# Optimization experiments

Measured on AMD Instinct MI355X. Metric: run time of the kernel, lower is better.

Reference implementation:

```python
import jax, jax.numpy as jnp
import numpy as np

B, S, DIM = 2, 2048, 2048
N_HEADS, N_KV_HEADS = 16, 4
HEAD_DIM = DIM // N_HEADS  # 128
N_REP = N_HEADS // N_KV_HEADS
ROPE_THETA = 10000.0


def _rope_cos_sin(bsz, seqlen, head_dim, theta):
    # precompute_freqs_cis (unscaled): angles[t, i] = t * theta^{-2i/d}
    inv_freq = 1.0 / (theta ** (np.arange(0, head_dim, 2)[: head_dim // 2].astype(np.float32) / head_dim))
    t = np.arange(seqlen, dtype=np.float32)
    ang = np.outer(t, inv_freq)  # [S, hd/2]
    cos = np.broadcast_to(np.cos(ang), (bsz, seqlen, head_dim // 2))
    sin = np.broadcast_to(np.sin(ang), (bsz, seqlen, head_dim // 2))
    return jnp.asarray(cos), jnp.asarray(sin)


def setup_inputs() -> dict:
    key = jax.random.key(0)
    ks = jax.random.split(key, 5)
    scale = 1.0 / np.sqrt(DIM)
    x = jax.random.normal(ks[0], (B, S, DIM), dtype=jnp.float32)
    wq = jax.random.normal(ks[1], (DIM, N_HEADS * HEAD_DIM), dtype=jnp.float32) * scale
    wk = jax.random.normal(ks[2], (DIM, N_KV_HEADS * HEAD_DIM), dtype=jnp.float32) * scale
    wv = jax.random.normal(ks[3], (DIM, N_KV_HEADS * HEAD_DIM), dtype=jnp.float32) * scale
    wo = jax.random.normal(ks[4], (N_HEADS * HEAD_DIM, DIM), dtype=jnp.float32) * scale
    freqs_cos, freqs_sin = _rope_cos_sin(B, S, HEAD_DIM, ROPE_THETA)
    return {"x": x, "wq": wq, "wk": wk, "wv": wv, "wo": wo,
            "freqs_cos": freqs_cos, "freqs_sin": freqs_sin}


def _apply_rope(t, cos, sin):
    # t: [B, S, H, hd]; cos/sin: [B, S, hd/2] -> complex mult on (even, odd) pairs
    tr = t.reshape(*t.shape[:-1], -1, 2)  # [B,S,H,hd/2,2]
    xr, xi = tr[..., 0], tr[..., 1]
    c = cos[:, :, None, :]
    s = sin[:, :, None, :]
    out_r = xr * c - xi * s
    out_i = xr * s + xi * c
    return jnp.stack([out_r, out_i], axis=-1).reshape(t.shape)


def reference(x, wq, wk, wv, wo, freqs_cos, freqs_sin):
    bsz, seqlen, _ = x.shape
    xq = (x @ wq).reshape(bsz, seqlen, N_HEADS, HEAD_DIM)
    xk = (x @ wk).reshape(bsz, seqlen, N_KV_HEADS, HEAD_DIM)
    xv = (x @ wv).reshape(bsz, seqlen, N_KV_HEADS, HEAD_DIM)

    xq = _apply_rope(xq, freqs_cos, freqs_sin)
    xk = _apply_rope(xk, freqs_cos, freqs_sin)

    # repeat_kv (GQA): [B,S,KV,hd] -> [B,S,H,hd]
    xk = jnp.repeat(xk, N_REP, axis=2)
    xv = jnp.repeat(xv, N_REP, axis=2)

    # [B,H,Sq,Sk]
    scores = jnp.einsum('bqhd,bkhd->bhqk', xq, xk) / np.sqrt(HEAD_DIM).astype(np.float32)
    # additive causal mask (triu of -inf, diagonal=1)
    causal = jnp.triu(jnp.full((seqlen, seqlen), -jnp.inf, dtype=scores.dtype), k=1)
    scores = scores + causal
    probs = jax.nn.softmax(scores.astype(jnp.float32), axis=-1).astype(xq.dtype)
    out = jnp.einsum('bhqk,bkhd->bqhd', probs, xv).reshape(bsz, seqlen, -1)
    return out @ wo
```

## Files before the change

kernel.cpp:

```cpp
#include <hip/hip_runtime.h>
#include <stdint.h>

#define SEQ   2048
#define NB    2
#define LDQKV 3072
#define HD    128
#define QSCALE2 (0.08838834764831845f * 1.44269504088896340f)

typedef __attribute__((ext_vector_type(8))) short short8;
typedef __attribute__((ext_vector_type(4))) short short4v;
typedef __attribute__((ext_vector_type(4))) float f32x4;
typedef __attribute__((ext_vector_type(16))) float f32x16;
typedef __attribute__((ext_vector_type(4))) unsigned int u32x4;
typedef __attribute__((ext_vector_type(2))) unsigned int u32x2;
typedef __attribute__((ext_vector_type(8))) __bf16 bf16x8;

__device__ __forceinline__ float bs2f(short s) {
  unsigned int u = ((unsigned int)(unsigned short)s) << 16;
  return __builtin_bit_cast(float, u);
}
__device__ __forceinline__ short f2bs(float f) {
  unsigned int u = __builtin_bit_cast(unsigned int, f);
  u += 0x7fffu + ((u >> 16) & 1u);
  return (short)(u >> 16);
}
__device__ __forceinline__ unsigned int cvt_pk(float lo, float hi) {
  unsigned int r;
  asm("v_cvt_pk_bf16_f32 %0, %1, %2" : "=v"(r) : "v"(lo), "v"(hi));
  return r;
}
__device__ __forceinline__ f32x4 mfma16(short8 a, short8 b, f32x4 c) {
  return __builtin_amdgcn_mfma_f32_16x16x32_bf16(
      __builtin_bit_cast(bf16x8, a), __builtin_bit_cast(bf16x8, b), c, 0, 0, 0);
}
__device__ __forceinline__ f32x16 mfma32(short8 a, short8 b, f32x16 c) {
  return __builtin_amdgcn_mfma_f32_32x32x16_bf16(
      __builtin_bit_cast(bf16x8, a), __builtin_bit_cast(bf16x8, b), c, 0, 0, 0);
}
__device__ __forceinline__ void gload_lds16(const void* g, void* l) {
  __builtin_amdgcn_global_load_lds(
      (__attribute__((address_space(1))) const void*)(uintptr_t)g,
      (__attribute__((address_space(3))) void*)(unsigned int)(uintptr_t)l,
      16, 0, 0);
}

#define SBAR() asm volatile("s_barrier" ::: "memory")
#define VMC4() asm volatile("s_waitcnt vmcnt(4)" ::: "memory")
#define VMC0() asm volatile("s_waitcnt vmcnt(0)" ::: "memory")

__global__ __launch_bounds__(256) void k_prep(const float* __restrict__ x,
                                              const float* __restrict__ wq,
                                              const float* __restrict__ wk,
                                              const float* __restrict__ wv,
                                              const float* __restrict__ wo,
                                              short* __restrict__ xb,
                                              short* __restrict__ wT,
                                              short* __restrict__ woT) {
  __shared__ __align__(16) float tile[64][68];
  const int bid = blockIdx.x, t = threadIdx.x;
  if (bid < 4096) {
    int i = bid * 256 + t;
    f32x4 a = *(const f32x4*)(x + (size_t)i * 8);
    f32x4 b = *(const f32x4*)(x + (size_t)i * 8 + 4);
    short8 o;
#pragma unroll
    for (int j = 0; j < 4; ++j) { o[j] = f2bs(a[j]); o[4 + j] = f2bs(b[j]); }
    *(short8*)(xb + (size_t)i * 8) = o;
    return;
  }
  const float* src;
  short* dst;
  int N, id;
  if (bid < 5120)      { id = bid - 4096; src = wq; dst = wT;                        N = 2048; }
  else if (bid < 5376) { id = bid - 5120; src = wk; dst = wT + (size_t)2048 * 2048;  N = 512;  }
  else if (bid < 5632) { id = bid - 5376; src = wv; dst = wT + (size_t)2560 * 2048;  N = 512;  }
  else                 { id = bid - 5632; src = wo; dst = woT;                       N = 2048; }
  const int K = 2048;
  int k0 = (id & 31) * 64, n0 = (id >> 5) * 64;
#pragma unroll
  for (int rep = 0; rep < 4; ++rep) {
    int lin = rep * 1024 + t * 4;
    int kk = lin >> 6, nn = lin & 63;
    f32x4 v = *(const f32x4*)(src + (size_t)(k0 + kk) * N + n0 + nn);
    *(f32x4*)(&tile[kk][nn]) = v;
  }
  __syncthreads();
#pragma unroll
  for (int rep = 0; rep < 4; ++rep) {
    int lin = rep * 1024 + t * 4;
    int nn = lin >> 6, kk = lin & 63;
    short4v o;
#pragma unroll
    for (int j = 0; j < 4; ++j) o[j] = f2bs(tile[kk + j][nn]);
    *(short4v*)(dst + (size_t)(n0 + nn) * K + k0 + kk) = o;
  }
}

template <int FP32OUT>
__global__ __launch_bounds__(512, 2) void k_gemm256(const short* __restrict__ A,
                                                    const short* __restrict__ Bt,
                                                    void* __restrict__ Cp,
                                                    int M, int N, int K) {
  __shared__ short Al[2][2][128 * 64];
  __shared__ short Bl[2][2][128 * 64];
  const int t = threadIdx.x, l = t & 63, w = t >> 6;
  const int pm = w >> 2, pn = w & 3;
  const int lrow = l & 15, lg = l >> 4;
  const int NT = K >> 6;

  const int nbm = M >> 8;
  const int per = gridDim.x >> 3;
  const int id2 = (blockIdx.x & 7) * per + (blockIdx.x >> 3);
  const int m0 = (id2 % nbm) * 256, n0 = (id2 / nbm) * 256;

  const int srow = w * 8 + (l >> 3);
  const int sgx = ((l & 7) ^ (srow & 7)) * 8;
  const short* Abase = A + (size_t)(m0 + srow) * K + sgx;
  const short* Bbase = Bt + (size_t)(n0 + srow) * K + sgx;

  f32x4 acc[8][4] = {};
  short8 aFr[4][2], bFr[2][2];

  auto stgA = [&](int d, int h, int tv) {
    const short* g = Abase + (size_t)(h * 128) * K + (size_t)tv * 64;
    gload_lds16(g, &Al[d][h][w * 512]);
    gload_lds16(g + (size_t)64 * K, &Al[d][h][w * 512 + 4096]);
  };
  auto stgB = [&](int d, int h, int tv) {
    const short* g = Bbase + (size_t)(h * 128) * K + (size_t)tv * 64;
    gload_lds16(g, &Bl[d][h][w * 512]);
    gload_lds16(g + (size_t)64 * K, &Bl[d][h][w * 512 + 4096]);
  };
  auto rdA = [&](int d, int Mh) {
#pragma unroll
    for (int mi = 0; mi < 4; ++mi) {
      int rl = pm * 64 + mi * 16 + lrow;
#pragma unroll
      for (int kk = 0; kk < 2; ++kk)
        aFr[mi][kk] = *(const short8*)&Al[d][Mh][rl * 64 +
                                                 (((kk * 4 + lg) ^ (rl & 7)) * 8)];
    }
  };
  auto rdB = [&](int d, int Nh) {
#pragma unroll
    for (int ni = 0; ni < 2; ++ni) {
      int rl = pn * 32 + ni * 16 + lrow;
#pragma unroll
      for (int kk = 0; kk < 2; ++kk)
        bFr[ni][kk] = *(const short8*)&Bl[d][Nh][rl * 64 +
                                                 (((kk * 4 + lg) ^ (rl & 7)) * 8)];
    }
  };

#define MMQ(Mh, Nh)                                                          \
  do {                                                                       \
    __builtin_amdgcn_s_setprio(1);                                           \
    _Pragma("unroll") for (int mi = 0; mi < 4; ++mi)                         \
        _Pragma("unroll") for (int ni = 0; ni < 2; ++ni)                     \
            _Pragma("unroll") for (int kk = 0; kk < 2; ++kk)                 \
                acc[(Mh)*4 + mi][(Nh)*2 + ni] =                              \
                    mfma16(aFr[mi][kk], bFr[ni][kk],                         \
                           acc[(Mh)*4 + mi][(Nh)*2 + ni]);                   \
    __builtin_amdgcn_s_setprio(0);                                           \
  } while (0)

  stgA(0, 0, 0); stgB(0, 0, 0); stgB(0, 1, 0); stgA(0, 1, 0);
  stgA(1, 0, 1); stgB(1, 1, 1);
  VMC4();
  SBAR();

  for (int v = 0; v < NT; ++v) {
    const int d = v & 1, d1 = d ^ 1;
    rdA(d, 0); rdB(d, 0);
    if (v + 1 < NT) stgB(d1, 0, v + 1);
    SBAR();
    MMQ(0, 0);
    rdB(d, 1);
    if (v + 1 < NT) stgA(d1, 1, v + 1);
    SBAR();
    MMQ(0, 1);
    rdA(d, 1);
    if (v + 2 < NT) stgA(d, 0, v + 2);
    SBAR();
    MMQ(1, 1);
    rdB(d, 0);
    if (v + 2 < NT) stgB(d, 1, v + 2);
    SBAR();
    MMQ(1, 0);
    if (v + 2 < NT) { VMC4(); } else { VMC0(); }
    SBAR();
  }
#undef MMQ

#pragma unroll
  for (int Mh = 0; Mh < 2; ++Mh)
#pragma unroll
    for (int mi = 0; mi < 4; ++mi)
#pragma unroll
      for (int Nh = 0; Nh < 2; ++Nh)
#pragma unroll
        for (int ni = 0; ni < 2; ++ni) {
          int row = m0 + Mh * 128 + pm * 64 + mi * 16 + lg * 4;
          int col = n0 + Nh * 128 + pn * 32 + ni * 16 + lrow;
          f32x4 vv = acc[Mh * 4 + mi][Nh * 2 + ni];
#pragma unroll
          for (int v2 = 0; v2 < 4; ++v2) {
            if constexpr (FP32OUT)
              ((float*)Cp)[(size_t)(row + v2) * N + col] = vv[v2];
            else
              ((short*)Cp)[(size_t)(row + v2) * N + col] = f2bs(vv[v2]);
          }
        }
}

__global__ __launch_bounds__(256) void k_rv(short* __restrict__ qkv,
                                            const float* __restrict__ fcos,
                                            const float* __restrict__ fsin,
                                            short* __restrict__ vt) {
  __shared__ short tile[128 * 137];
  const int bid = blockIdx.x, t = threadIdx.x;
  if (bid < 5120) {
    int tid = bid * 256 + t;
    int p16 = tid & 15;
    int slice = (tid >> 4) % 20;
    int bs = tid / 320;
    int col = (slice < 16) ? slice * 128 + p16 * 8
                           : 2048 + (slice - 16) * 128 + p16 * 8;
    short8 x = *(short8*)(qkv + (size_t)bs * LDQKV + col);
    f32x4 c = *(const f32x4*)(fcos + (size_t)bs * 64 + p16 * 4);
    f32x4 s = *(const f32x4*)(fsin + (size_t)bs * 64 + p16 * 4);
    float sc = (slice < 16) ? QSCALE2 : 1.0f;
    short8 o;
#pragma unroll
    for (int j = 0; j < 4; ++j) {
      float xr = bs2f(x[2 * j]), xi = bs2f(x[2 * j + 1]);
      o[2 * j] = f2bs((xr * c[j] - xi * s[j]) * sc);
      o[2 * j + 1] = f2bs((xr * s[j] + xi * c[j]) * sc);
    }
    *(short8*)(qkv + (size_t)bs * LDQKV + col) = o;
    return;
  }
  const int id = bid - 5120;
  int s0 = (id & 15) * 128;
  int kvh = (id >> 4) & 3, b = id >> 6;
  const short* src = qkv + (size_t)(b * SEQ) * LDQKV + 2560 + kvh * 128;
#pragma unroll
  for (int rep = 0; rep < 8; ++rep) {
    int lin = rep * 2048 + t * 8;
    int si = lin >> 7, d = lin & 127;
    short8 v = *(const short8*)(src + (size_t)(s0 + si) * LDQKV + d);
#pragma unroll
    for (int j = 0; j < 8; ++j) tile[si * 137 + d + j] = v[j];
  }
  __syncthreads();
  short* dst = vt + (size_t)((b * 4 + kvh) * 128) * SEQ;
#pragma unroll
  for (int rep = 0; rep < 8; ++rep) {
    int lin = rep * 2048 + t * 8;
    int d = lin >> 7, sb = lin & 127;
    short8 o;
#pragma unroll
    for (int j = 0; j < 8; ++j) o[j] = tile[(sb + j) * 137 + d];
    *(short8*)(dst + (size_t)d * SEQ + s0 + sb) = o;
  }
}

__global__ __launch_bounds__(256, 2) void k_attn(const short* __restrict__ qkv,
                                                 const short* __restrict__ vt,
                                                 short* __restrict__ outp) {
  __shared__ short Ks[2][64 * 128];
  __shared__ short Vs[2][128 * 64];
  const int t = threadIdx.x, l = t & 63, w = t >> 6;
  const int wr = w >> 1, wk = w & 1;
  const int h = blockIdx.y, b = blockIdx.z;
  const int kvh = h >> 2;
  const int lo5 = l & 31, hi = l >> 5;

  const int kkey = t >> 4, kd8 = t & 15;
  const int vdd = t >> 3, vs8 = t & 7;
  const short* kbase = qkv + (size_t)(b * SEQ) * LDQKV + 2048 + kvh * HD;
  const short* vbase = vt + (size_t)((b * 4 + kvh) * 128) * SEQ;

  auto stageKV = [&](int buf, int it) {
    const int kt = it * 64;
    short* kdst = &Ks[buf][w * 512];
    short* vdst = &Vs[buf][w * 512];
#pragma unroll
    for (int i = 0; i < 4; ++i) {
      int key = i * 16 + kkey;
      int sd = (kd8 ^ (key & 15)) * 8;
      gload_lds16(kbase + (size_t)(kt + key) * LDQKV + sd, kdst + i * 2048);
    }
#pragma unroll
    for (int i = 0; i < 4; ++i) {
      int d = i * 32 + vdd;
      int ss = (vs8 ^ (d & 7)) * 8;
      gload_lds16(vbase + (size_t)d * SEQ + kt + ss, vdst + i * 2048);
    }
  };

  int koff[8], voff[4][2];
#pragma unroll
  for (int s = 0; s < 8; ++s)
    koff[s] = (wk * 32 + lo5) * 128 + (((hi + 2 * s) ^ (l & 15)) * 8);
#pragma unroll
  for (int db = 0; db < 4; ++db)
#pragma unroll
    for (int s = 0; s < 2; ++s)
      voff[db][s] =
          (db * 32 + lo5) * 64 + (((4 * wk + hi + 2 * s) ^ (l & 7)) * 8);
  const int kbloc = wk * 32 + 4 * hi;
  const int qloc = wr * 32 + lo5;

  for (int part = 0; part < 2; ++part) {
    const int qt = part ? (31 - (int)blockIdx.x) : (int)blockIdx.x;
    const int q0 = qt * 64;

    short8 qf[8];
    {
      const short* qrow =
          qkv + (size_t)(b * SEQ + q0 + wr * 32 + lo5) * LDQKV + h * HD;
#pragma unroll
      for (int s = 0; s < 8; ++s)
        qf[s] = *(const short8*)(qrow + s * 16 + hi * 8);
    }

    f32x16 of[4] = {};
    float mrun = 0.f, lsum = 0.f;

    const int nt = qt + 1;
    stageKV(0, 0);
    __syncthreads();

    for (int it = 0; it < nt; ++it) {
      const int buf = it & 1;
      if (it + 1 < nt) stageKV(buf ^ 1, it + 1);
      const short* KsC = Ks[buf];
      const short* VsC = Vs[buf];

      f32x16 sc = {};
      __builtin_amdgcn_s_setprio(1);
#pragma unroll
      for (int s = 0; s < 8; ++s) {
        short8 kf = *(const short8*)(KsC + koff[s]);
        sc = mfma32(kf, qf[s], sc);
      }
      __builtin_amdgcn_s_setprio(0);

      if (it == nt - 1) {
#pragma unroll
        for (int r = 0; r < 16; ++r) {
          const int off = (r & 3) + 8 * (r >> 2);
          if (kbloc + off > qloc) sc[r] = -1e30f;
        }
      }

      float lmax = sc[0];
#pragma unroll
      for (int r = 1; r < 16; ++r) lmax = fmaxf(lmax, sc[r]);
      if (__any(lmax > mrun + 8.f)) {
        float mx = fmaxf(lmax, __shfl_xor(lmax, 32));
        float mm = fmaxf(mrun, mx);
        float rs = exp2f(mrun - mm);
        mrun = mm;
        lsum *= rs;
#pragma unroll
        for (int db = 0; db < 4; ++db)
#pragma unroll
          for (int r = 0; r < 16; ++r) of[db][r] *= rs;
      }

      float p[16];
#pragma unroll
      for (int r = 0; r < 16; ++r) {
        p[r] = exp2f(sc[r] - mrun);
        lsum += p[r];
      }
      unsigned int pk[8];
#pragma unroll
      for (int j = 0; j < 8; ++j) pk[j] = cvt_pk(p[2 * j], p[2 * j + 1]);

      unsigned int s0 = hi ? pk[0] : pk[2];
      unsigned int s1 = hi ? pk[1] : pk[3];
      unsigned int s2 = hi ? pk[4] : pk[6];
      unsigned int s3 = hi ? pk[5] : pk[7];
      unsigned int x0 = __shfl_xor(s0, 32);
      unsigned int x1 = __shfl_xor(s1, 32);
      unsigned int x2 = __shfl_xor(s2, 32);
      unsigned int x3 = __shfl_xor(s3, 32);
      u32x4 b0w, b1w;
      b0w.x = hi ? x0 : pk[0];
      b0w.y = hi ? x1 : pk[1];
      b0w.z = hi ? pk[2] : x0;
      b0w.w = hi ? pk[3] : x1;
      b1w.x = hi ? x2 : pk[4];
      b1w.y = hi ? x3 : pk[5];
      b1w.z = hi ? pk[6] : x2;
      b1w.w = hi ? pk[7] : x3;
      short8 pb[2] = {__builtin_bit_cast(short8, b0w),
                      __builtin_bit_cast(short8, b1w)};

      __builtin_amdgcn_s_setprio(1);
#pragma unroll
      for (int s = 0; s < 2; ++s)
#pragma unroll
        for (int db = 0; db < 4; ++db) {
          short8 vf = *(const short8*)(VsC + voff[db][s]);
          of[db] = mfma32(vf, pb[s], of[db]);
        }
      __builtin_amdgcn_s_setprio(0);
      __syncthreads();
    }

    lsum += __shfl_xor(lsum, 32);
    float* og = (float*)Ks;
    float* sg = (float*)Vs;
    if (wk == 1) {
#pragma unroll
      for (int db = 0; db < 4; ++db)
#pragma unroll
        for (int r4 = 0; r4 < 4; ++r4) {
          int g = db * 4 + r4;
          f32x4 v;
#pragma unroll
          for (int j = 0; j < 4; ++j) v[j] = of[db][r4 * 4 + j];
          *(f32x4*)&og[wr * 4096 + l * 64 + ((g ^ (l & 15)) * 4)] = v;
        }
      sg[wr * 64 + l] = mrun;
      sg[128 + wr * 64 + l] = lsum;
    }
    __syncthreads();
    if (wk == 0) {
      float m1 = sg[wr * 64 + l];
      float l1 = sg[128 + wr * 64 + l];
      float mt = fmaxf(mrun, m1);
      float r0 = exp2f(mrun - mt), r1 = exp2f(m1 - mt);
      float inv = 1.0f / (lsum * r0 + l1 * r1);
      short* ob =
          outp + (size_t)(b * SEQ + q0 + wr * 32 + lo5) * 2048 + h * HD;
#pragma unroll
      for (int db = 0; db < 4; ++db) {
#pragma unroll
        for (int r4 = 0; r4 < 4; ++r4) {
          int g = db * 4 + r4;
          f32x4 o1 = *(const f32x4*)&og[wr * 4096 + l * 64 +
                                        ((g ^ (l & 15)) * 4)];
          u32x2 pko;
          float v0 = (of[db][r4 * 4 + 0] * r0 + o1[0] * r1) * inv;
          float v1 = (of[db][r4 * 4 + 1] * r0 + o1[1] * r1) * inv;
          float v2 = (of[db][r4 * 4 + 2] * r0 + o1[2] * r1) * inv;
          float v3 = (of[db][r4 * 4 + 3] * r0 + o1[3] * r1) * inv;
          pko.x = cvt_pk(v0, v1);
          pko.y = cvt_pk(v2, v3);
          *(u32x2*)(ob + db * 32 + 8 * r4 + 4 * hi) = pko;
        }
      }
    }
    __syncthreads();
  }
}

extern "C" void kernel_launch(void* const* d_in, const int* in_sizes, int n_in,
                              void* d_out, int out_size, void* d_ws,
                              size_t ws_size, hipStream_t stream) {
  const float* x = (const float*)d_in[0];
  const float* wq = (const float*)d_in[1];
  const float* wk = (const float*)d_in[2];
  const float* wv = (const float*)d_in[3];
  const float* wo = (const float*)d_in[4];
  const float* fc = (const float*)d_in[5];
  const float* fs = (const float*)d_in[6];

  char* ws = (char*)d_ws;
  short* xb = (short*)(ws);
  short* wT = (short*)(ws + (16ull << 20));
  short* woT = (short*)(ws + (28ull << 20));
  short* qkvb = (short*)(ws + (36ull << 20));
  short* vtb = (short*)(ws + (16ull << 20));
  short* attn = (short*)(ws);

  k_prep<<<6656, 256, 0, stream>>>(x, wq, wk, wv, wo, xb, wT, woT);
  k_gemm256<0><<<192, 512, 0, stream>>>(xb, wT, qkvb, 4096, 3072, 2048);
  k_rv<<<5248, 256, 0, stream>>>(qkvb, fc, fs, vtb);
  k_attn<<<dim3(16, 16, 2), 256, 0, stream>>>(qkvb, vtb, attn);
  k_gemm256<1><<<128, 512, 0, stream>>>(attn, woT, d_out, 4096, 2048, 2048);
}
```

Before: 205.3 us.

## Template GEMM on N-tile width and restructure k-loop into two half-phases

The GEMM kernel is templated on the number of 128-wide N halves, so the output projection uses 256x128 tiles with 256 blocks instead of 128 blocks of 256x256, which puts more blocks across the CUs. The main loop now reads all A and B fragments up front, issues the next stages' loads, and runs the MFMA work in two halves with two barriers per k-step instead of four. The cost is extra fragment registers (two A fragment sets), which may limit occupancy, and the smaller N tile gives less reuse of A.

```diff
diff --git a/kernel.cpp b/kernel.cpp
--- a/kernel.cpp
+++ b/kernel.cpp
@@ -45,8 +45,7 @@
 }
 
 #define SBAR() asm volatile("s_barrier" ::: "memory")
-#define VMC4() asm volatile("s_waitcnt vmcnt(4)" ::: "memory")
-#define VMC0() asm volatile("s_waitcnt vmcnt(0)" ::: "memory")
+#define VMC(n) asm volatile("s_waitcnt vmcnt(" #n ")" ::: "memory")
 
 __global__ __launch_bounds__(256) void k_prep(const float* __restrict__ x,
                                               const float* __restrict__ wq,
@@ -96,13 +95,13 @@
   }
 }
 
-template <int FP32OUT>
+template <int NH, int FP32OUT>
 __global__ __launch_bounds__(512, 2) void k_gemm256(const short* __restrict__ A,
                                                     const short* __restrict__ Bt,
                                                     void* __restrict__ Cp,
                                                     int M, int N, int K) {
   __shared__ short Al[2][2][128 * 64];
-  __shared__ short Bl[2][2][128 * 64];
+  __shared__ short Bl[2][NH][128 * 64];
   const int t = threadIdx.x, l = t & 63, w = t >> 6;
   const int pm = w >> 2, pn = w & 3;
   const int lrow = l & 15, lg = l >> 4;
@@ -111,15 +110,15 @@
   const int nbm = M >> 8;
   const int per = gridDim.x >> 3;
   const int id2 = (blockIdx.x & 7) * per + (blockIdx.x >> 3);
-  const int m0 = (id2 % nbm) * 256, n0 = (id2 / nbm) * 256;
+  const int m0 = (id2 % nbm) * 256, n0 = (id2 / nbm) * (NH * 128);
 
   const int srow = w * 8 + (l >> 3);
   const int sgx = ((l & 7) ^ (srow & 7)) * 8;
   const short* Abase = A + (size_t)(m0 + srow) * K + sgx;
   const short* Bbase = Bt + (size_t)(n0 + srow) * K + sgx;
 
-  f32x4 acc[8][4] = {};
-  short8 aFr[4][2], bFr[2][2];
+  f32x4 acc[8][NH * 2] = {};
+  short8 aFr0[4][2], aFr1[4][2], bFr[NH][2][2];
 
   auto stgA = [&](int d, int h, int tv) {
     const short* g = Abase + (size_t)(h * 128) * K + (size_t)tv * 64;
@@ -131,78 +130,84 @@
     gload_lds16(g, &Bl[d][h][w * 512]);
     gload_lds16(g + (size_t)64 * K, &Bl[d][h][w * 512 + 4096]);
   };
-  auto rdA = [&](int d, int Mh) {
+  auto rdA = [&](int d, int Mh, short8 (*dst)[2]) {
 #pragma unroll
     for (int mi = 0; mi < 4; ++mi) {
       int rl = pm * 64 + mi * 16 + lrow;
 #pragma unroll
       for (int kk = 0; kk < 2; ++kk)
-        aFr[mi][kk] = *(const short8*)&Al[d][Mh][rl * 64 +
+        dst[mi][kk] = *(const short8*)&Al[d][Mh][rl * 64 +
                                                  (((kk * 4 + lg) ^ (rl & 7)) * 8)];
     }
   };
-  auto rdB = [&](int d, int Nh) {
-#pragma unroll
-    for (int ni = 0; ni < 2; ++ni) {
-      int rl = pn * 32 + ni * 16 + lrow;
-#pragma unroll
-      for (int kk = 0; kk < 2; ++kk)
-        bFr[ni][kk] = *(const short8*)&Bl[d][Nh][rl * 64 +
-                                                 (((kk * 4 + lg) ^ (rl & 7)) * 8)];
-    }
+  auto rdB = [&](int d) {
+#pragma unroll
+    for (int h = 0; h < NH; ++h)
+#pragma unroll
+      for (int ni = 0; ni < 2; ++ni) {
+        int rl = pn * 32 + ni * 16 + lrow;
+#pragma unroll
+        for (int kk = 0; kk < 2; ++kk)
+          bFr[h][ni][kk] =
+              *(const short8*)&Bl[d][h][rl * 64 +
+                                        (((kk * 4 + lg) ^ (rl & 7)) * 8)];
+      }
   };
 
-#define MMQ(Mh, Nh)                                                          \
+#define MMH(Mh, FR)                                                          \
   do {                                                                       \
     __builtin_amdgcn_s_setprio(1);                                           \
-    _Pragma("unroll") for (int mi = 0; mi < 4; ++mi)                         \
-        _Pragma("unroll") for (int ni = 0; ni < 2; ++ni)                     \
-            _Pragma("unroll") for (int kk = 0; kk < 2; ++kk)                 \
-                acc[(Mh)*4 + mi][(Nh)*2 + ni] =                              \
-                    mfma16(aFr[mi][kk], bFr[ni][kk],                         \
-                           acc[(Mh)*4 + mi][(Nh)*2 + ni]);                   \
+    _Pragma("unroll") for (int h = 0; h < NH; ++h)                           \
+        _Pragma("unroll") for (int mi = 0; mi < 4; ++mi)                     \
+            _Pragma("unroll") for (int ni = 0; ni < 2; ++ni)                 \
+                _Pragma("unroll") for (int kk = 0; kk < 2; ++kk)             \
+                    acc[(Mh)*4 + mi][h * 2 + ni] =                           \
+                        mfma16(FR[mi][kk], bFr[h][ni][kk],                   \
+                               acc[(Mh)*4 + mi][h * 2 + ni]);                \
     __builtin_amdgcn_s_setprio(0);                                           \
   } while (0)
 
-  stgA(0, 0, 0); stgB(0, 0, 0); stgB(0, 1, 0); stgA(0, 1, 0);
-  stgA(1, 0, 1); stgB(1, 1, 1);
-  VMC4();
+  stgA(0, 0, 0);
+  for (int h = 0; h < NH; ++h) stgB(0, h, 0);
+  stgA(0, 1, 0);
+  stgA(1, 0, 1);
+  if (NH == 2) stgB(1, 1, 1);
+  if (NH == 2) { VMC(4); } else { VMC(2); }
   SBAR();
 
   for (int v = 0; v < NT; ++v) {
     const int d = v & 1, d1 = d ^ 1;
-    rdA(d, 0); rdB(d, 0);
-    if (v + 1 < NT) stgB(d1, 0, v + 1);
+    rdA(d, 0, aFr0);
+    rdB(d);
+    rdA(d, 1, aFr1);
+    if (v + 1 < NT) { stgB(d1, 0, v + 1); stgA(d1, 1, v + 1); }
+    MMH(0, aFr0);
     SBAR();
-    MMQ(0, 0);
-    rdB(d, 1);
-    if (v + 1 < NT) stgA(d1, 1, v + 1);
+    if (v + 2 < NT) {
+      stgA(d, 0, v + 2);
+      if (NH == 2) stgB(d, 1, v + 2);
+    }
+    MMH(1, aFr1);
+    if (v + 2 < NT) {
+      if (NH == 2) { VMC(4); } else { VMC(2); }
+    } else {
+      VMC(0);
+    }
     SBAR();
-    MMQ(0, 1);
-    rdA(d, 1);
-    if (v + 2 < NT) stgA(d, 0, v + 2);
-    SBAR();
-    MMQ(1, 1);
-    rdB(d, 0);
-    if (v + 2 < NT) stgB(d, 1, v + 2);
-    SBAR();
-    MMQ(1, 0);
-    if (v + 2 < NT) { VMC4(); } else { VMC0(); }
-    SBAR();
-  }
-#undef MMQ
+  }
+#undef MMH
 
 #pragma unroll
   for (int Mh = 0; Mh < 2; ++Mh)
 #pragma unroll
     for (int mi = 0; mi < 4; ++mi)
 #pragma unroll
-      for (int Nh = 0; Nh < 2; ++Nh)
+      for (int h = 0; h < NH; ++h)
 #pragma unroll
         for (int ni = 0; ni < 2; ++ni) {
           int row = m0 + Mh * 128 + pm * 64 + mi * 16 + lg * 4;
-          int col = n0 + Nh * 128 + pn * 32 + ni * 16 + lrow;
-          f32x4 vv = acc[Mh * 4 + mi][Nh * 2 + ni];
+          int col = n0 + h * 128 + pn * 32 + ni * 16 + lrow;
+          f32x4 vv = acc[Mh * 4 + mi][h * 2 + ni];
 #pragma unroll
           for (int v2 = 0; v2 < 4; ++v2) {
             if constexpr (FP32OUT)
@@ -480,8 +485,8 @@
   short* attn = (short*)(ws);
 
   k_prep<<<6656, 256, 0, stream>>>(x, wq, wk, wv, wo, xb, wT, woT);
-  k_gemm256<0><<<192, 512, 0, stream>>>(xb, wT, qkvb, 4096, 3072, 2048);
+  k_gemm256<2, 0><<<192, 512, 0, stream>>>(xb, wT, qkvb, 4096, 3072, 2048);
   k_rv<<<5248, 256, 0, stream>>>(qkvb, fc, fs, vtb);
   k_attn<<<dim3(16, 16, 2), 256, 0, stream>>>(qkvb, vtb, attn);
-  k_gemm256<1><<<128, 512, 0, stream>>>(attn, woT, d_out, 4096, 2048, 2048);
-}
+  k_gemm256<1, 1><<<256, 512, 0, stream>>>(attn, woT, d_out, 4096, 2048, 2048);
+}
```

Measured after the change: 189.9 us. 1.08x faster.
